# Optimization experiments

Hardware: AMD Instinct MI355X
Metric: run time of the kernel (lower is better)

The kernel has to match this reference:

```python
import jax, jax.numpy as jnp
import numpy as np
from jax import lax

B, S, L, E, H, V = 32, 64, 256, 64, 64, 6000


def setup_inputs() -> dict:
    key = jax.random.key(0)
    ks = jax.random.split(key, 8)
    inp = {
        "ids": jax.random.randint(ks[0], (B, S, L), 0, V, dtype=jnp.int32),
        "embed_table": jax.random.normal(ks[1], (V, E), jnp.float32) * 0.05,
        "Wk_f": jax.random.normal(ks[2], (E, 4 * H), jnp.float32) * 0.05,
        "Wr_f": jax.random.normal(ks[3], (H, 4 * H), jnp.float32) * 0.05,
        "b_f": jnp.zeros((4 * H,), jnp.float32),
        "Wk_b": jax.random.normal(ks[4], (E, 4 * H), jnp.float32) * 0.05,
        "Wr_b": jax.random.normal(ks[5], (H, 4 * H), jnp.float32) * 0.05,
        "b_b": jnp.zeros((4 * H,), jnp.float32),
    }
    return inp


def _lstm(xs, Wk, Wr, b):
    # xs: [L, N, E] -> hidden states [L, N, H]; Keras LSTM gate order i,f,c,o
    N = xs.shape[1]
    Hh = Wr.shape[0]
    pre = jnp.einsum('lne,eg->lng', xs, Wk) + b  # input projection once, outside scan

    def step(carry, zt):
        h, c = carry
        z = zt + h @ Wr
        i, f, g, o = jnp.split(z, 4, axis=-1)
        i = jax.nn.sigmoid(i)
        f = jax.nn.sigmoid(f)
        g = jnp.tanh(g)
        o = jax.nn.sigmoid(o)
        c = f * c + i * g
        h = o * jnp.tanh(c)
        return (h, c), h

    h0 = jnp.zeros((N, Hh), xs.dtype)
    _, hs = lax.scan(step, (h0, h0), pre)
    return hs


def reference(ids, embed_table, Wk_f, Wr_f, b_f, Wk_b, Wr_b, b_b):
    b, s, l = ids.shape
    e = embed_table.shape[1]
    h = Wr_f.shape[0]
    x = embed_table[ids]                      # [B,S,L,E]
    xs = x.reshape(b * s, l, e).transpose(1, 0, 2)  # [L, B*S, E]
    h_fwd = _lstm(xs, Wk_f, Wr_f, b_f)              # [L, N, H]
    h_bwd = _lstm(xs[::-1], Wk_b, Wr_b, b_b)[::-1]  # [L, N, H]
    out = jnp.concatenate([h_fwd, h_bwd], axis=-1)  # [L, N, 2H]
    return out.transpose(1, 0, 2).reshape(b, s, l, 2 * h)
```

## Files before the change

kernel.cpp:

```cpp
#include <hip/hip_runtime.h>

#define LL 256
#define EE 64
#define HH 64
#define GG 256
#define VV 6000
#define NSEQ 16
#define ROWP 72
#define VBLK 375

typedef __bf16 bf16_t;
typedef bf16_t bf16x8 __attribute__((ext_vector_type(8)));
typedef float  f32x4  __attribute__((ext_vector_type(4)));

union BfPack {
    unsigned short u[8];
    bf16x8 v;
};

__device__ __forceinline__ unsigned short f2bf(float f) {
    return __builtin_bit_cast(unsigned short, (__bf16)f);
}

#define LOG2E 1.44269504088896340736f

__device__ __forceinline__ float sigm(float x) {
    float e = __builtin_amdgcn_exp2f(-LOG2E * x);
    return __builtin_amdgcn_rcpf(1.0f + e);
}
__device__ __forceinline__ float tanh_fast(float x) {
    float e = __builtin_amdgcn_exp2f((2.0f * LOG2E) * x);
    return 1.0f - 2.0f * __builtin_amdgcn_rcpf(e + 1.0f);
}

#define LGKM_BARRIER() asm volatile("s_waitcnt lgkmcnt(0)\n\ts_barrier" ::: "memory")

__global__ __launch_bounds__(256)
void embed_pre_kernel(const float* __restrict__ embed,
                      const float* __restrict__ Wk_f, const float* __restrict__ b_f,
                      const float* __restrict__ Wk_b, const float* __restrict__ b_b,
                      unsigned short* __restrict__ pre)
{
    const int bid = blockIdx.x;
    const int dir = bid / VBLK;
    const int v0  = (bid % VBLK) * 16;
    const float* Wk = dir ? Wk_b : Wk_f;
    const float* bv = dir ? b_b  : b_f;
    unsigned short* dst = pre + (size_t)dir * VV * GG;

    const int tid = threadIdx.x;
    const int r   = tid >> 4;
    const int cg  = tid & 15;

    __shared__ float sW[16][GG];
    __shared__ float sE[16][17];

    float acc[16];
    #pragma unroll
    for (int k = 0; k < 16; ++k) acc[k] = 0.f;

    for (int ec = 0; ec < 4; ++ec) {
        {
            int er = tid >> 4;
            int c0 = (tid & 15) * 16;
            const float* src = &Wk[(size_t)(ec * 16 + er) * GG + c0];
            *(float4*)&sW[er][c0 + 0]  = *(const float4*)(src + 0);
            *(float4*)&sW[er][c0 + 4]  = *(const float4*)(src + 4);
            *(float4*)&sW[er][c0 + 8]  = *(const float4*)(src + 8);
            *(float4*)&sW[er][c0 + 12] = *(const float4*)(src + 12);
            sE[er][tid & 15] = embed[(size_t)(v0 + er) * EE + ec * 16 + (tid & 15)];
        }
        __syncthreads();
        #pragma unroll
        for (int e = 0; e < 16; ++e) {
            float xe = sE[r][e];
            #pragma unroll
            for (int k = 0; k < 16; ++k)
                acc[k] += xe * sW[e][k * 16 + cg];
        }
        __syncthreads();
    }
    #pragma unroll
    for (int a = 0; a < 4; ++a) {
        ushort4 pk;
        pk.x = f2bf(acc[a]      + bv[(a)      * 16 + cg]);
        pk.y = f2bf(acc[a + 4]  + bv[(a + 4)  * 16 + cg]);
        pk.z = f2bf(acc[a + 8]  + bv[(a + 8)  * 16 + cg]);
        pk.w = f2bf(acc[a + 12] + bv[(a + 12) * 16 + cg]);
        *(ushort4*)&dst[(size_t)(v0 + r) * GG + a * 64 + cg * 4] = pk;
    }
}

__global__ __launch_bounds__(256, 1)
void bilstm_mfma(const int* __restrict__ ids,
                 const float* __restrict__ Wr_f, const float* __restrict__ Wr_b,
                 const unsigned short* __restrict__ pre,
                 float* __restrict__ out)
{
    const int dir = blockIdx.x >> 7;
    const int grp = blockIdx.x & 127;
    const int n0  = grp * NSEQ;
    const int tid  = threadIdx.x;
    const int w    = tid >> 6;
    const int lane = tid & 63;
    const int l15  = lane & 15;
    const int quad = lane >> 4;
    const int j    = w * 16 + l15;

    const float* Wr = dir ? Wr_b : Wr_f;
    const unsigned short* preT = pre + (size_t)dir * VV * GG;
    const int coff = w * 64 + l15 * 4;

    __shared__ __align__(16) short s_h[2][NSEQ][ROWP];
    __shared__ int s_ids[NSEQ][LL + 1];

    for (int p = tid; p < NSEQ * LL; p += 256) {
        int m = p >> 8, t = p & 255;
        s_ids[m][t] = ids[(size_t)(n0 + m) * LL + t];
    }
    for (int p = tid; p < 2 * NSEQ * ROWP; p += 256)
        (&s_h[0][0][0])[p] = 0;

    __syncthreads();

    bf16x8 bfrag[4][2];
    #pragma unroll
    for (int tt = 0; tt < 4; ++tt) {
        int g = tt * 64 + j;
        #pragma unroll
        for (int kc = 0; kc < 2; ++kc) {
            BfPack pk;
            #pragma unroll
            for (int e = 0; e < 8; ++e) {
                int kg = kc * 32 + quad * 8 + e;
                pk.u[e] = f2bf(Wr[(size_t)kg * GG + g]);
            }
            bfrag[tt][kc] = pk.v;
        }
    }

    uint2 PA[4], PB[4];
    {
        int t0 = dir ? (LL - 1) : 0;
        int t1 = dir ? (LL - 2) : 1;
        #pragma unroll
        for (int r = 0; r < 4; ++r) {
            PA[r] = *(const uint2*)&preT[(size_t)s_ids[quad * 4 + r][t0] * GG + coff];
            PB[r] = *(const uint2*)&preT[(size_t)s_ids[quad * 4 + r][t1] * GG + coff];
        }
    }

    float c[4] = {0.f, 0.f, 0.f, 0.f};

    const int tstep = dir ? -(2 * HH) : (2 * HH);
    float* optr[4];
    {
        const int t0 = dir ? (LL - 1) : 0;
        #pragma unroll
        for (int r = 0; r < 4; ++r)
            optr[r] = out + ((size_t)(n0 + quad * 4 + r) * LL + t0) * (2 * HH) + dir * HH + j;
    }

    auto do_step = [&](int ts, uint2 (&P)[4]) {
        const int rb = ts & 1, wb = (ts + 1) & 1;

        bf16x8 ah0 = *(const bf16x8*)&s_h[rb][l15][quad * 8];
        bf16x8 ah1 = *(const bf16x8*)&s_h[rb][l15][32 + quad * 8];

        f32x4 cIn[4];
        #pragma unroll
        for (int r = 0; r < 4; ++r) {
            cIn[0][r] = __uint_as_float(P[r].x << 16);
            cIn[1][r] = __uint_as_float(P[r].x & 0xffff0000u);
            cIn[2][r] = __uint_as_float(P[r].y << 16);
            cIn[3][r] = __uint_as_float(P[r].y & 0xffff0000u);
        }

        {
            int tn = dir ? (LL - 3 - ts) : (ts + 2);
            tn = tn < 0 ? 0 : (tn > LL - 1 ? LL - 1 : tn);
            #pragma unroll
            for (int r = 0; r < 4; ++r)
                P[r] = *(const uint2*)&preT[(size_t)s_ids[quad * 4 + r][tn] * GG + coff];
        }

        f32x4 acc[4];
        #pragma unroll
        for (int tt = 0; tt < 4; ++tt) {
            f32x4 a = __builtin_amdgcn_mfma_f32_16x16x32_bf16(ah0, bfrag[tt][0], cIn[tt], 0, 0, 0);
            acc[tt]  = __builtin_amdgcn_mfma_f32_16x16x32_bf16(ah1, bfrag[tt][1], a, 0, 0, 0);
        }

        #pragma unroll
        for (int r = 0; r < 4; ++r) {
            float ig = sigm(acc[0][r]);
            float fg = sigm(acc[1][r]);
            float gg = tanh_fast(acc[2][r]);
            float og = sigm(acc[3][r]);
            c[r] = fg * c[r] + ig * gg;
            float hh = og * tanh_fast(c[r]);
            *optr[r] = hh;
            optr[r] += tstep;
            s_h[wb][quad * 4 + r][j] = (short)f2bf(hh);
        }

        LGKM_BARRIER();
    };

    for (int ts = 0; ts < LL; ts += 2) {
        do_step(ts,     PA);
        do_step(ts + 1, PB);
    }
}

extern "C" void kernel_launch(void* const* d_in, const int* in_sizes, int n_in,
                              void* d_out, int out_size, void* d_ws, size_t ws_size,
                              hipStream_t stream) {
    const int*   ids   = (const int*)d_in[0];
    const float* embed = (const float*)d_in[1];
    const float* Wk_f  = (const float*)d_in[2];
    const float* Wr_f  = (const float*)d_in[3];
    const float* b_f   = (const float*)d_in[4];
    const float* Wk_b  = (const float*)d_in[5];
    const float* Wr_b  = (const float*)d_in[6];
    const float* b_b   = (const float*)d_in[7];
    float* out = (float*)d_out;
    unsigned short* pre = (unsigned short*)d_ws;

    embed_pre_kernel<<<dim3(2 * VBLK), dim3(256), 0, stream>>>(
        embed, Wk_f, b_f, Wk_b, b_b, pre);

    bilstm_mfma<<<dim3(256), dim3(256), 0, stream>>>(ids, Wr_f, Wr_b, pre, out);
}
```

Measured before the change: 405.5 us.

## Split LSTM gate nonlinearities across extra waves via LDS handoff

Doubles the block to 512 threads. Four waves run the recurrent MFMAs and then hand half of each accumulator tile (rows 2-3) through shared memory to four helper waves. Each wave then evaluates the sigmoid/tanh cell update and writes output for only two rows instead of four. This shortens the serial elementwise tail of each timestep, at the cost of an extra barrier and an LDS round trip per step.

```diff
diff --git a/kernel.cpp b/kernel.cpp
--- a/kernel.cpp
+++ b/kernel.cpp
@@ -91,7 +91,7 @@
     }
 }
 
-__global__ __launch_bounds__(256, 1)
+__global__ __launch_bounds__(512, 2)
 void bilstm_mfma(const int* __restrict__ ids,
                  const float* __restrict__ Wr_f, const float* __restrict__ Wr_b,
                  const unsigned short* __restrict__ pre,
@@ -102,45 +102,47 @@
     const int n0  = grp * NSEQ;
     const int tid  = threadIdx.x;
     const int w    = tid >> 6;
+    const int w0   = w & 3;
+    const int role = w >> 2;
     const int lane = tid & 63;
     const int l15  = lane & 15;
     const int quad = lane >> 4;
-    const int j    = w * 16 + l15;
+    const int j    = w0 * 16 + l15;
 
     const float* Wr = dir ? Wr_b : Wr_f;
     const unsigned short* preT = pre + (size_t)dir * VV * GG;
-    const int coff = w * 64 + l15 * 4;
+    const int coff = w0 * 64 + l15 * 4;
 
     __shared__ __align__(16) short s_h[2][NSEQ][ROWP];
     __shared__ int s_ids[NSEQ][LL + 1];
-
-    for (int p = tid; p < NSEQ * LL; p += 256) {
+    __shared__ float s_xacc[8][256];
+
+    for (int p = tid; p < NSEQ * LL; p += 512) {
         int m = p >> 8, t = p & 255;
         s_ids[m][t] = ids[(size_t)(n0 + m) * LL + t];
     }
-    for (int p = tid; p < 2 * NSEQ * ROWP; p += 256)
+    for (int p = tid; p < 2 * NSEQ * ROWP; p += 512)
         (&s_h[0][0][0])[p] = 0;
 
     __syncthreads();
 
     bf16x8 bfrag[4][2];
-    #pragma unroll
-    for (int tt = 0; tt < 4; ++tt) {
-        int g = tt * 64 + j;
-        #pragma unroll
-        for (int kc = 0; kc < 2; ++kc) {
-            BfPack pk;
-            #pragma unroll
-            for (int e = 0; e < 8; ++e) {
-                int kg = kc * 32 + quad * 8 + e;
-                pk.u[e] = f2bf(Wr[(size_t)kg * GG + g]);
-            }
-            bfrag[tt][kc] = pk.v;
-        }
-    }
-
     uint2 PA[4], PB[4];
-    {
+    if (role == 0) {
+        #pragma unroll
+        for (int tt = 0; tt < 4; ++tt) {
+            int g = tt * 64 + j;
+            #pragma unroll
+            for (int kc = 0; kc < 2; ++kc) {
+                BfPack pk;
+                #pragma unroll
+                for (int e = 0; e < 8; ++e) {
+                    int kg = kc * 32 + quad * 8 + e;
+                    pk.u[e] = f2bf(Wr[(size_t)kg * GG + g]);
+                }
+                bfrag[tt][kc] = pk.v;
+            }
+        }
         int t0 = dir ? (LL - 1) : 0;
         int t1 = dir ? (LL - 2) : 1;
         #pragma unroll
@@ -150,60 +152,81 @@
         }
     }
 
-    float c[4] = {0.f, 0.f, 0.f, 0.f};
+    float c[2] = {0.f, 0.f};
+    const int rowb = quad * 4 + role * 2;
 
     const int tstep = dir ? -(2 * HH) : (2 * HH);
-    float* optr[4];
+    float* optr[2];
     {
         const int t0 = dir ? (LL - 1) : 0;
         #pragma unroll
-        for (int r = 0; r < 4; ++r)
-            optr[r] = out + ((size_t)(n0 + quad * 4 + r) * LL + t0) * (2 * HH) + dir * HH + j;
+        for (int rr = 0; rr < 2; ++rr)
+            optr[rr] = out + ((size_t)(n0 + rowb + rr) * LL + t0) * (2 * HH) + dir * HH + j;
     }
 
     auto do_step = [&](int ts, uint2 (&P)[4]) {
         const int rb = ts & 1, wb = (ts + 1) & 1;
 
-        bf16x8 ah0 = *(const bf16x8*)&s_h[rb][l15][quad * 8];
-        bf16x8 ah1 = *(const bf16x8*)&s_h[rb][l15][32 + quad * 8];
-
-        f32x4 cIn[4];
-        #pragma unroll
-        for (int r = 0; r < 4; ++r) {
-            cIn[0][r] = __uint_as_float(P[r].x << 16);
-            cIn[1][r] = __uint_as_float(P[r].x & 0xffff0000u);
-            cIn[2][r] = __uint_as_float(P[r].y << 16);
-            cIn[3][r] = __uint_as_float(P[r].y & 0xffff0000u);
-        }
-
-        {
-            int tn = dir ? (LL - 3 - ts) : (ts + 2);
-            tn = tn < 0 ? 0 : (tn > LL - 1 ? LL - 1 : tn);
-            #pragma unroll
-            for (int r = 0; r < 4; ++r)
-                P[r] = *(const uint2*)&preT[(size_t)s_ids[quad * 4 + r][tn] * GG + coff];
-        }
-
         f32x4 acc[4];
-        #pragma unroll
-        for (int tt = 0; tt < 4; ++tt) {
-            f32x4 a = __builtin_amdgcn_mfma_f32_16x16x32_bf16(ah0, bfrag[tt][0], cIn[tt], 0, 0, 0);
-            acc[tt]  = __builtin_amdgcn_mfma_f32_16x16x32_bf16(ah1, bfrag[tt][1], a, 0, 0, 0);
-        }
-
-        #pragma unroll
-        for (int r = 0; r < 4; ++r) {
-            float ig = sigm(acc[0][r]);
-            float fg = sigm(acc[1][r]);
-            float gg = tanh_fast(acc[2][r]);
-            float og = sigm(acc[3][r]);
-            c[r] = fg * c[r] + ig * gg;
-            float hh = og * tanh_fast(c[r]);
-            *optr[r] = hh;
-            optr[r] += tstep;
-            s_h[wb][quad * 4 + r][j] = (short)f2bf(hh);
-        }
-
+        if (role == 0) {
+            bf16x8 ah0 = *(const bf16x8*)&s_h[rb][l15][quad * 8];
+            bf16x8 ah1 = *(const bf16x8*)&s_h[rb][l15][32 + quad * 8];
+
+            f32x4 cIn[4];
+            #pragma unroll
+            for (int r = 0; r < 4; ++r) {
+                cIn[0][r] = __uint_as_float(P[r].x << 16);
+                cIn[1][r] = __uint_as_float(P[r].x & 0xffff0000u);
+                cIn[2][r] = __uint_as_float(P[r].y << 16);
+                cIn[3][r] = __uint_as_float(P[r].y & 0xffff0000u);
+            }
+            {
+                int tn = dir ? (LL - 3 - ts) : (ts + 2);
+                tn = tn < 0 ? 0 : (tn > LL - 1 ? LL - 1 : tn);
+                #pragma unroll
+                for (int r = 0; r < 4; ++r)
+                    P[r] = *(const uint2*)&preT[(size_t)s_ids[quad * 4 + r][tn] * GG + coff];
+            }
+            #pragma unroll
+            for (int tt = 0; tt < 4; ++tt) {
+                f32x4 a = __builtin_amdgcn_mfma_f32_16x16x32_bf16(ah0, bfrag[tt][0], cIn[tt], 0, 0, 0);
+                acc[tt]  = __builtin_amdgcn_mfma_f32_16x16x32_bf16(ah1, bfrag[tt][1], a, 0, 0, 0);
+            }
+            #pragma unroll
+            for (int tt = 0; tt < 4; ++tt) {
+                s_xacc[tt * 2 + 0][w0 * 64 + lane] = acc[tt][2];
+                s_xacc[tt * 2 + 1][w0 * 64 + lane] = acc[tt][3];
+            }
+        }
+        LGKM_BARRIER();
+
+        float z[4][2];
+        if (role == 0) {
+            #pragma unroll
+            for (int tt = 0; tt < 4; ++tt) {
+                z[tt][0] = acc[tt][0];
+                z[tt][1] = acc[tt][1];
+            }
+        } else {
+            #pragma unroll
+            for (int tt = 0; tt < 4; ++tt) {
+                z[tt][0] = s_xacc[tt * 2 + 0][w0 * 64 + lane];
+                z[tt][1] = s_xacc[tt * 2 + 1][w0 * 64 + lane];
+            }
+        }
+
+        #pragma unroll
+        for (int rr = 0; rr < 2; ++rr) {
+            float ig = sigm(z[0][rr]);
+            float fg = sigm(z[1][rr]);
+            float gg = tanh_fast(z[2][rr]);
+            float og = sigm(z[3][rr]);
+            c[rr] = fg * c[rr] + ig * gg;
+            float hh = og * tanh_fast(c[rr]);
+            *optr[rr] = hh;
+            optr[rr] += tstep;
+            s_h[wb][rowb + rr][j] = (short)f2bf(hh);
+        }
         LGKM_BARRIER();
     };
 
@@ -230,5 +253,5 @@
     embed_pre_kernel<<<dim3(2 * VBLK), dim3(256), 0, stream>>>(
         embed, Wk_f, b_f, Wk_b, b_b, pre);
 
-    bilstm_mfma<<<dim3(256), dim3(256), 0, stream>>>(ids, Wr_f, Wr_b, pre, out);
-}
+    bilstm_mfma<<<dim3(256), dim3(512), 0, stream>>>(ids, Wr_f, Wr_b, pre, out);
+}
```

Measured after the change: 412.4 us. Within noise of the previous version (+1.7%).

## Pack forward and backward directions into one block's MFMA rows

Applied to the files above, without the earlier changes.

Each block now handles 8 sequences in both directions instead of 16 sequences in one direction. The 16 MFMA rows are split so the first half carries forward-direction sequences and the second half carries backward ones. Each step runs the recurrent matmul against both weight sets and picks per row the result matching its direction. This keeps the grid size the same but doubles the MFMA count per step and the register footprint for weight fragments, and half of that matmul work is thrown away.

```diff
diff --git a/kernel.cpp b/kernel.cpp
--- a/kernel.cpp
+++ b/kernel.cpp
@@ -4,8 +4,8 @@
 #define EE 64
 #define HH 64
 #define GG 256
+#define NSEQ 8
 #define VV 6000
-#define NSEQ 16
 #define ROWP 72
 #define VBLK 375
 
@@ -97,8 +97,7 @@
                  const unsigned short* __restrict__ pre,
                  float* __restrict__ out)
 {
-    const int dir = blockIdx.x >> 7;
-    const int grp = blockIdx.x & 127;
+    const int grp = blockIdx.x;
     const int n0  = grp * NSEQ;
     const int tid  = threadIdx.x;
     const int w    = tid >> 6;
@@ -106,59 +105,64 @@
     const int l15  = lane & 15;
     const int quad = lane >> 4;
     const int j    = w * 16 + l15;
-
-    const float* Wr = dir ? Wr_b : Wr_f;
-    const unsigned short* preT = pre + (size_t)dir * VV * GG;
+    const int dirq = quad >> 1;
+    const int seqb = (quad & 1) * 4;
+
+    const unsigned short* preT = pre + (size_t)dirq * VV * GG;
     const int coff = w * 64 + l15 * 4;
 
-    __shared__ __align__(16) short s_h[2][NSEQ][ROWP];
+    __shared__ __align__(16) short s_h[2][16][ROWP];
     __shared__ int s_ids[NSEQ][LL + 1];
 
     for (int p = tid; p < NSEQ * LL; p += 256) {
         int m = p >> 8, t = p & 255;
         s_ids[m][t] = ids[(size_t)(n0 + m) * LL + t];
     }
-    for (int p = tid; p < 2 * NSEQ * ROWP; p += 256)
+    for (int p = tid; p < 2 * 16 * ROWP; p += 256)
         (&s_h[0][0][0])[p] = 0;
 
     __syncthreads();
 
-    bf16x8 bfrag[4][2];
+    bf16x8 bfrag[2][4][2];
     #pragma unroll
-    for (int tt = 0; tt < 4; ++tt) {
-        int g = tt * 64 + j;
-        #pragma unroll
-        for (int kc = 0; kc < 2; ++kc) {
-            BfPack pk;
+    for (int d = 0; d < 2; ++d) {
+        const float* Wr = d ? Wr_b : Wr_f;
+        #pragma unroll
+        for (int tt = 0; tt < 4; ++tt) {
+            int g = tt * 64 + j;
             #pragma unroll
-            for (int e = 0; e < 8; ++e) {
-                int kg = kc * 32 + quad * 8 + e;
-                pk.u[e] = f2bf(Wr[(size_t)kg * GG + g]);
+            for (int kc = 0; kc < 2; ++kc) {
+                BfPack pk;
+                #pragma unroll
+                for (int e = 0; e < 8; ++e) {
+                    int kg = kc * 32 + quad * 8 + e;
+                    pk.u[e] = f2bf(Wr[(size_t)kg * GG + g]);
+                }
+                bfrag[d][tt][kc] = pk.v;
             }
-            bfrag[tt][kc] = pk.v;
         }
     }
 
     uint2 PA[4], PB[4];
     {
-        int t0 = dir ? (LL - 1) : 0;
-        int t1 = dir ? (LL - 2) : 1;
+        int tA = dirq ? (LL - 1) : 0;
+        int tB = dirq ? (LL - 2) : 1;
         #pragma unroll
         for (int r = 0; r < 4; ++r) {
-            PA[r] = *(const uint2*)&preT[(size_t)s_ids[quad * 4 + r][t0] * GG + coff];
-            PB[r] = *(const uint2*)&preT[(size_t)s_ids[quad * 4 + r][t1] * GG + coff];
+            PA[r] = *(const uint2*)&preT[(size_t)s_ids[seqb + r][tA] * GG + coff];
+            PB[r] = *(const uint2*)&preT[(size_t)s_ids[seqb + r][tB] * GG + coff];
         }
     }
 
     float c[4] = {0.f, 0.f, 0.f, 0.f};
 
-    const int tstep = dir ? -(2 * HH) : (2 * HH);
+    const int tstep = dirq ? -(2 * HH) : (2 * HH);
     float* optr[4];
     {
-        const int t0 = dir ? (LL - 1) : 0;
+        const int t0 = dirq ? (LL - 1) : 0;
         #pragma unroll
         for (int r = 0; r < 4; ++r)
-            optr[r] = out + ((size_t)(n0 + quad * 4 + r) * LL + t0) * (2 * HH) + dir * HH + j;
+            optr[r] = out + ((size_t)(n0 + seqb + r) * LL + t0) * (2 * HH) + dirq * HH + j;
     }
 
     auto do_step = [&](int ts, uint2 (&P)[4]) {
@@ -175,28 +179,33 @@
             cIn[2][r] = __uint_as_float(P[r].y << 16);
             cIn[3][r] = __uint_as_float(P[r].y & 0xffff0000u);
         }
-
         {
-            int tn = dir ? (LL - 3 - ts) : (ts + 2);
+            int tn = dirq ? (LL - 3 - ts) : (ts + 2);
             tn = tn < 0 ? 0 : (tn > LL - 1 ? LL - 1 : tn);
             #pragma unroll
             for (int r = 0; r < 4; ++r)
-                P[r] = *(const uint2*)&preT[(size_t)s_ids[quad * 4 + r][tn] * GG + coff];
-        }
-
-        f32x4 acc[4];
+                P[r] = *(const uint2*)&preT[(size_t)s_ids[seqb + r][tn] * GG + coff];
+        }
+
+        f32x4 accF[4], accB[4];
         #pragma unroll
         for (int tt = 0; tt < 4; ++tt) {
-            f32x4 a = __builtin_amdgcn_mfma_f32_16x16x32_bf16(ah0, bfrag[tt][0], cIn[tt], 0, 0, 0);
-            acc[tt]  = __builtin_amdgcn_mfma_f32_16x16x32_bf16(ah1, bfrag[tt][1], a, 0, 0, 0);
+            f32x4 af = __builtin_amdgcn_mfma_f32_16x16x32_bf16(ah0, bfrag[0][tt][0], cIn[tt], 0, 0, 0);
+            accF[tt]  = __builtin_amdgcn_mfma_f32_16x16x32_bf16(ah1, bfrag[0][tt][1], af, 0, 0, 0);
+            f32x4 ab = __builtin_amdgcn_mfma_f32_16x16x32_bf16(ah0, bfrag[1][tt][0], cIn[tt], 0, 0, 0);
+            accB[tt]  = __builtin_amdgcn_mfma_f32_16x16x32_bf16(ah1, bfrag[1][tt][1], ab, 0, 0, 0);
         }
 
         #pragma unroll
         for (int r = 0; r < 4; ++r) {
-            float ig = sigm(acc[0][r]);
-            float fg = sigm(acc[1][r]);
-            float gg = tanh_fast(acc[2][r]);
-            float og = sigm(acc[3][r]);
+            float zi = dirq ? accB[0][r] : accF[0][r];
+            float zf = dirq ? accB[1][r] : accF[1][r];
+            float zg = dirq ? accB[2][r] : accF[2][r];
+            float zo = dirq ? accB[3][r] : accF[3][r];
+            float ig = sigm(zi);
+            float fg = sigm(zf);
+            float gg = tanh_fast(zg);
+            float og = sigm(zo);
             c[r] = fg * c[r] + ig * gg;
             float hh = og * tanh_fast(c[r]);
             *optr[r] = hh;
```

Result: slower. 434.7 us (+7.2%).
